# Kernel optimization log

Measured on AMD Instinct MI355X. Metric: run time of the kernel, lower is better.

The kernel has to match this reference:

```python
import jax, jax.numpy as jnp
import numpy as np

B, QL, VL, HID, NH, CH = 16, 512, 512, 1024, 4, 10
DIM = HID // NH  # 256


def setup_inputs() -> dict:
    key = jax.random.key(0)
    ks = jax.random.split(key, 16)
    n = lambda k, s, sc=0.02: jax.random.normal(k, s, jnp.float32) * sc
    return {
        "query": jax.random.normal(ks[0], (B, QL, HID), jnp.float32),
        "value": jax.random.normal(ks[1], (B, VL, HID), jnp.float32),
        "prev_attn": jax.nn.softmax(jax.random.normal(ks[2], (B * NH, VL), jnp.float32), axis=-1),
        "conv_w": n(ks[3], (CH, 1, 3)),          # conv1d weight (out, in, k)
        "conv_b": jnp.zeros((CH,), jnp.float32),
        "Wq": n(ks[4], (HID, HID)), "bq": jnp.zeros((HID,), jnp.float32),  # query_projection
        "Wv": n(ks[5], (HID, HID)),               # value_projection (no bias)
        "Wloc": n(ks[6], (CH, DIM)),              # loc_projection (no bias)
        "bias": jax.random.uniform(ks[7], (HID,), jnp.float32, -0.1, 0.1),
        "Wout": n(ks[8], (2 * HID, HID)), "bout": jnp.zeros((HID,), jnp.float32),
        "swq": n(ks[9], (DIM, DIM)), "sbq": jnp.zeros((DIM,), jnp.float32),
        "swk": n(ks[10], (DIM, DIM)), "sbk": jnp.zeros((DIM,), jnp.float32),
        "swv": n(ks[11], (DIM, DIM)), "sbv": jnp.zeros((DIM,), jnp.float32),
    }


def _forward(query, value, prev_attn, conv_w, conv_b, Wq, bq, Wv, Wloc, bias,
             Wout, bout, swq, sbq, swk, sbk, swv, sbv):
    # location energy: conv1d over prev alignment, then per-head linear
    conv = jax.lax.conv_general_dilated(
        prev_attn[:, None, :], conv_w, window_strides=(1,), padding=((1, 1),),
        dimension_numbers=("NCH", "OIH", "NCH")) + conv_b[None, :, None]  # (B*NH, CH, VL)
    conv = conv.reshape(B, NH, CH, VL).transpose(0, 1, 3, 2)              # (B, NH, VL, CH)
    loc = jnp.einsum("bhvc,cd->bhvd", conv, Wloc)                         # (B, NH, VL, DIM)
    loc = loc.transpose(0, 2, 1, 3).reshape(B, VL, HID)                   # (B, VL, HID)

    q = query @ Wq + bq                                                   # (B, QL, HID)
    v = value @ Wv + loc + bias                                           # (B, VL, HID)

    # split heads: (B, L, NH, DIM) -> (NH*B, L, DIM)
    qh = q.reshape(B, QL, NH, DIM).transpose(2, 0, 1, 3).reshape(NH * B, QL, DIM)
    vh = v.reshape(B, VL, NH, DIM).transpose(2, 0, 1, 3).reshape(NH * B, VL, DIM)

    # scaled dot-product attention with key = value = vh (intended call)
    qq = qh @ swq + sbq
    kk = vh @ swk + sbk
    vv = vh @ swv + sbv
    scores = jnp.einsum("nqd,nkd->nqk", qq, kk) / np.float32(np.sqrt(DIM))
    attn = jax.nn.softmax(scores, axis=-1)                                # (NH*B, QL, VL)
    ctx = jnp.einsum("nqk,nkd->nqd", attn, vv)

    # merge heads: (NH, B, QL, DIM) -> (B, QL, HID)
    ctx = ctx.reshape(NH, B, QL, DIM).transpose(1, 2, 0, 3).reshape(B, QL, HID)

    combined = jnp.concatenate([ctx, query], axis=2)                      # (B, QL, 2*HID)
    out = jnp.tanh(combined @ Wout + bout)                                # (B, QL, HID)
    return out, attn


def reference(query, value, prev_attn, conv_w, conv_b, Wq, bq, Wv, Wloc, bias,
              Wout, bout, swq, sbq, swk, sbk, swv, sbv):
    return _forward(query, value, prev_attn, conv_w, conv_b, Wq, bq, Wv, Wloc,
                    bias, Wout, bout, swq, sbq, swk, sbk, swv, sbv)
```

## Files before the change

kernel.cpp:

```cpp
#include <hip/hip_runtime.h>
#include <math.h>

#define B_   16
#define QL_  512
#define VL_  512
#define HID_ 1024
#define NH_  4
#define CH_  10
#define DIM_ 256

typedef __attribute__((ext_vector_type(4))) float f32x4;
typedef __attribute__((ext_vector_type(8))) short bf16x8;

__device__ __forceinline__ ushort f2bf(float f) {
    union { float f; uint32_t u; } c; c.f = f;
    uint32_t u = c.u;
    u += 0x7fffu + ((u >> 16) & 1u);
    return (ushort)(u >> 16);
}

__device__ __forceinline__ void gload16(const void* g, void* l) {
    __builtin_amdgcn_global_load_lds((const __attribute__((address_space(1))) void*)g,
                                     (__attribute__((address_space(3))) void*)l,
                                     16, 0, 0);
}

__global__ __launch_bounds__(256)
void gemm_bf16(const ushort* __restrict__ A, const ushort* __restrict__ Bt,
               void* __restrict__ Cv, void* __restrict__ Cv2,
               const float* __restrict__ bias,
               int K, int lda, int ldb, int ldc,
               long long a1, long long a2, long long b1, long long b2,
               long long c1, long long c2, int WB,
               float post_scale, int flags)
{
    __shared__ ushort As[2][128 * 64];
    __shared__ ushort Bs[2][128 * 64];

    int z = blockIdx.z;
    int zm = z % WB, zd = z / WB;
    A  += a1 * zm + a2 * zd;
    Bt += b1 * zm + b2 * zd;
    long long coff = c1 * (long long)zm + c2 * (long long)zd;

    int gx = gridDim.x;
    int nwg = gx * gridDim.y;
    int flat = blockIdx.y * gx + blockIdx.x;
    int q = nwg >> 3, r = nwg & 7;
    int xcd = flat & 7, idx = flat >> 3;
    int logical = (xcd < r ? xcd * (q + 1) : r * (q + 1) + (xcd - r) * q) + idx;
    int brow = (logical / gx) * 128;
    int bcol = (logical % gx) * 128;

    int t = threadIdx.x;
    int lane = t & 63, w = t >> 6;
    int wr = (w >> 1) * 64, wc = (w & 1) * 64;

    int srow  = t >> 3;
    int sslot = t & 7;
    int sk = ((sslot ^ (srow & 7)) << 3);
    const ushort* gaBase = A  + (long long)(brow + srow) * lda + sk;
    const ushort* gbBase = Bt + (long long)(bcol + srow) * ldb + sk;

    f32x4 acc[4][4] = {};

    auto stage = [&](int buf, int k0) {
        ushort* la = &As[buf][t * 8];
        ushort* lb = &Bs[buf][t * 8];
        #pragma unroll
        for (int i = 0; i < 4; ++i) {
            gload16(gaBase + (long long)(i * 32) * lda + k0, la + i * 2048);
            gload16(gbBase + (long long)(i * 32) * ldb + k0, lb + i * 2048);
        }
    };

    int NT = K >> 6;
    stage(0, 0);
    int cur = 0;
    for (int tI = 0; tI < NT; ++tI) {
        if (tI + 1 < NT) {
            stage(cur ^ 1, (tI + 1) << 6);
            asm volatile("s_waitcnt vmcnt(8)" ::: "memory");
        } else {
            asm volatile("s_waitcnt vmcnt(0)" ::: "memory");
        }
        __builtin_amdgcn_s_barrier();
        __builtin_amdgcn_sched_barrier(0);

        #pragma unroll
        for (int kk = 0; kk < 2; ++kk) {
            int slot = ((kk << 2) + (lane >> 4)) ^ (lane & 7);
            const ushort* ab = &As[cur][(wr + (lane & 15)) * 64 + slot * 8];
            const ushort* bb = &Bs[cur][(wc + (lane & 15)) * 64 + slot * 8];
            bf16x8 af[4], bfr[4];
            #pragma unroll
            for (int m = 0; m < 4; ++m) af[m]  = *(const bf16x8*)(ab + m * 1024);
            #pragma unroll
            for (int n = 0; n < 4; ++n) bfr[n] = *(const bf16x8*)(bb + n * 1024);
            #pragma unroll
            for (int m = 0; m < 4; ++m)
                #pragma unroll
                for (int n = 0; n < 4; ++n)
                    acc[m][n] = __builtin_amdgcn_mfma_f32_16x16x32_bf16(af[m], bfr[n], acc[m][n], 0, 0, 0);
        }

        __builtin_amdgcn_s_barrier();
        __builtin_amdgcn_sched_barrier(0);
        cur ^= 1;
    }

    float*  Cf = (float*)Cv + coff;
    ushort* Cb = (ushort*)Cv + coff;
    ushort* C2 = (ushort*)Cv2;
    #pragma unroll
    for (int m = 0; m < 4; ++m) {
        int r0 = brow + wr + m * 16 + (lane >> 4) * 4;
        #pragma unroll
        for (int n = 0; n < 4; ++n) {
            int c = bcol + wc + n * 16 + (lane & 15);
            float bv = bias ? bias[c] : 0.0f;
            float v0 = (acc[m][n][0] + bv) * post_scale;
            float v1 = (acc[m][n][1] + bv) * post_scale;
            float v2 = (acc[m][n][2] + bv) * post_scale;
            float v3 = (acc[m][n][3] + bv) * post_scale;
            if (flags & 2) { v0 = tanhf(v0); v1 = tanhf(v1); v2 = tanhf(v2); v3 = tanhf(v3); }
            if ((flags & 8) && c >= 1024) {
                ushort4 o;
                o.x = f2bf(v0); o.y = f2bf(v1); o.z = f2bf(v2); o.w = f2bf(v3);
                *(ushort4*)&C2[(long long)(c - 1024) * 8192 + r0] = o;
            } else if (flags & 1) {
                Cb[(long long)(r0 + 0) * ldc + c] = f2bf(v0);
                Cb[(long long)(r0 + 1) * ldc + c] = f2bf(v1);
                Cb[(long long)(r0 + 2) * ldc + c] = f2bf(v2);
                Cb[(long long)(r0 + 3) * ldc + c] = f2bf(v3);
            } else {
                Cf[(long long)(r0 + 0) * ldc + c] = v0;
                Cf[(long long)(r0 + 1) * ldc + c] = v1;
                Cf[(long long)(r0 + 2) * ldc + c] = v2;
                Cf[(long long)(r0 + 3) * ldc + c] = v3;
            }
        }
    }
}

__global__ __launch_bounds__(512, 1)
void scores_softmax(const ushort* __restrict__ qq, const ushort* __restrict__ kk,
                    float* __restrict__ attn, ushort* __restrict__ attnb)
{
    __shared__ ushort As[128 * 32];
    __shared__ ushort Bs[512 * 32];
    __shared__ float redm[4][128];
    __shared__ float reds[4][128];

    int z = blockIdx.z;
    int b = z & 15, h = z >> 4;
    const ushort* Abase = qq + (long long)b * 524288 + h * 256;
    const ushort* Bbase = kk + (long long)b * 524288 + h * 256;
    float*  aout = attn  + (long long)z * 262144;
    ushort* bout = attnb + (long long)z * 262144;

    int brow = blockIdx.y * 128;

    int t = threadIdx.x;
    int lane = t & 63, w = t >> 6;
    int wr = (w >> 2) * 64;
    int wc = (w & 3) * 128;

    int srow = t >> 2, sslot = t & 3;
    int sk = ((sslot ^ ((srow >> 1) & 3)) << 3);
    const ushort* ga = Abase + (long long)(brow + srow) * 1024 + sk;
    const ushort* gb = Bbase + (long long)srow * 1024 + sk;

    f32x4 acc[4][8] = {};

    for (int k0 = 0; k0 < 256; k0 += 32) {
        gload16(ga + k0, &As[t * 8]);
        #pragma unroll
        for (int i = 0; i < 4; ++i)
            gload16(gb + (long long)(i * 128) * 1024 + k0, &Bs[t * 8 + i * 4096]);
        __syncthreads();

        int slot = (lane >> 4) ^ ((lane >> 1) & 3);
        const ushort* ab = &As[(wr + (lane & 15)) * 32 + slot * 8];
        const ushort* bb = &Bs[(wc + (lane & 15)) * 32 + slot * 8];
        bf16x8 af[4], bfr[8];
        #pragma unroll
        for (int m = 0; m < 4; ++m) af[m]  = *(const bf16x8*)(ab + m * 512);
        #pragma unroll
        for (int n = 0; n < 8; ++n) bfr[n] = *(const bf16x8*)(bb + n * 512);
        #pragma unroll
        for (int m = 0; m < 4; ++m)
            #pragma unroll
            for (int n = 0; n < 8; ++n)
                acc[m][n] = __builtin_amdgcn_mfma_f32_16x16x32_bf16(af[m], bfr[n], acc[m][n], 0, 0, 0);
        __syncthreads();
    }

    float rmax[4][4], rinv[4][4];
    #pragma unroll
    for (int m = 0; m < 4; ++m)
        #pragma unroll
        for (int j = 0; j < 4; ++j) {
            float pm = acc[m][0][j];
            #pragma unroll
            for (int n = 1; n < 8; ++n) pm = fmaxf(pm, acc[m][n][j]);
            pm = fmaxf(pm, __shfl_xor(pm, 1));
            pm = fmaxf(pm, __shfl_xor(pm, 2));
            pm = fmaxf(pm, __shfl_xor(pm, 4));
            pm = fmaxf(pm, __shfl_xor(pm, 8));
            if ((lane & 15) == 0)
                redm[w & 3][wr + m * 16 + (lane >> 4) * 4 + j] = pm;
        }
    __syncthreads();
    #pragma unroll
    for (int m = 0; m < 4; ++m)
        #pragma unroll
        for (int j = 0; j < 4; ++j) {
            int row = wr + m * 16 + (lane >> 4) * 4 + j;
            rmax[m][j] = fmaxf(fmaxf(redm[0][row], redm[1][row]),
                               fmaxf(redm[2][row], redm[3][row]));
        }
    #pragma unroll
    for (int m = 0; m < 4; ++m)
        #pragma unroll
        for (int j = 0; j < 4; ++j) {
            float ps = 0.f;
            #pragma unroll
            for (int n = 0; n < 8; ++n) {
                float e = __expf(acc[m][n][j] - rmax[m][j]);
                acc[m][n][j] = e;
                ps += e;
            }
            ps += __shfl_xor(ps, 1);
            ps += __shfl_xor(ps, 2);
            ps += __shfl_xor(ps, 4);
            ps += __shfl_xor(ps, 8);
            if ((lane & 15) == 0)
                reds[w & 3][wr + m * 16 + (lane >> 4) * 4 + j] = ps;
        }
    __syncthreads();
    #pragma unroll
    for (int m = 0; m < 4; ++m)
        #pragma unroll
        for (int j = 0; j < 4; ++j) {
            int row = wr + m * 16 + (lane >> 4) * 4 + j;
            rinv[m][j] = 1.0f / (reds[0][row] + reds[1][row] + reds[2][row] + reds[3][row]);
        }
    #pragma unroll
    for (int m = 0; m < 4; ++m) {
        int r0 = brow + wr + m * 16 + (lane >> 4) * 4;
        #pragma unroll
        for (int n = 0; n < 8; ++n) {
            int c = wc + n * 16 + (lane & 15);
            #pragma unroll
            for (int j = 0; j < 4; ++j) {
                float v = acc[m][n][j] * rinv[m][j];
                aout[(long long)(r0 + j) * 512 + c] = v;
                bout[(long long)(r0 + j) * 512 + c] = f2bf(v);
            }
        }
    }
}

__global__ __launch_bounds__(256)
void vext_fill_conv(const float* __restrict__ prev, const float* __restrict__ cw,
                    const float* __restrict__ cb, ushort* __restrict__ vext)
{
    int idx = blockIdx.x * 256 + threadIdx.x;
    int row = idx >> 6, j = idx & 63;
    int b = row >> 9, l = row & 511;
    ushort v = 0;
    if (j < 40) {
        int h = j / 10, c = j - h * 10;
        const float* p = prev + (long long)(b * 4 + h) * VL_;
        float xm = (l > 0)       ? p[l - 1] : 0.f;
        float x0 = p[l];
        float xp = (l < VL_ - 1) ? p[l + 1] : 0.f;
        v = f2bf(xm * cw[c * 3 + 0] + x0 * cw[c * 3 + 1] + xp * cw[c * 3 + 2] + cb[c]);
    }
    vext[(long long)row * 1088 + 1024 + j] = v;
}

__global__ __launch_bounds__(256)
void fold_small(const float* __restrict__ bq, const float* __restrict__ sbq, const float* __restrict__ swq,
                const float* __restrict__ bias, const float* __restrict__ sbk, const float* __restrict__ swk,
                const float* __restrict__ sbv, const float* __restrict__ swv,
                const float* __restrict__ Wloc,
                float* __restrict__ bqq, float* __restrict__ bkv,
                float* __restrict__ wlK, float* __restrict__ wlV)
{
    int idx = blockIdx.x * 256 + threadIdx.x;
    if (idx < 1024) {
        int h = idx >> 8, d = idx & 255;
        float s = 0.f;
        for (int j = 0; j < 256; ++j) s += bq[h * 256 + j] * swq[j * 256 + d];
        bqq[idx] = s + sbq[d];
    } else if (idx < 3072) {
        int i = idx - 1024;
        int kv = i >> 10, ii = i & 1023;
        int h = ii >> 8, d = ii & 255;
        const float* sw = kv ? swv : swk;
        const float* sb = kv ? sbv : sbk;
        float s = 0.f;
        for (int j = 0; j < 256; ++j) s += bias[h * 256 + j] * sw[j * 256 + d];
        bkv[i] = s + sb[d];
    } else if (idx < 5632) {
        int i = idx - 3072; int c = i >> 8, d = i & 255;
        float s = 0.f;
        for (int j = 0; j < 256; ++j) s += Wloc[c * 256 + j] * swk[j * 256 + d];
        wlK[i] = s;
    } else if (idx < 8192) {
        int i = idx - 5632; int c = i >> 8, d = i & 255;
        float s = 0.f;
        for (int j = 0; j < 256; ++j) s += Wloc[c * 256 + j] * swv[j * 256 + d];
        wlV[i] = s;
    }
}

__global__ __launch_bounds__(256)
void cast_rows(const float* __restrict__ in, ushort* __restrict__ out, int ld_out)
{
    long long idx = (long long)blockIdx.x * 256 + threadIdx.x;
    long long row = idx >> 8;
    int c4 = (int)(idx & 255) * 4;
    float4 v = *(const float4*)&in[row * 1024 + c4];
    ushort4 o;
    o.x = f2bf(v.x); o.y = f2bf(v.y); o.z = f2bf(v.z); o.w = f2bf(v.w);
    *(ushort4*)&out[row * ld_out + c4] = o;
}

__global__ __launch_bounds__(256)
void transpose_cast(const float* __restrict__ in, ushort* __restrict__ out, int R, int C, int ld_out)
{
    __shared__ float tile[64][65];
    int r0 = blockIdx.y * 64, c0 = blockIdx.x * 64;
    int t = threadIdx.x;
    int tr = t >> 2, tc = (t & 3) * 16;
    const float* ip = in + (long long)(r0 + tr) * C + c0 + tc;
    #pragma unroll
    for (int i = 0; i < 4; ++i) {
        float4 v = *(const float4*)(ip + i * 4);
        tile[tr][tc + i * 4 + 0] = v.x;
        tile[tr][tc + i * 4 + 1] = v.y;
        tile[tr][tc + i * 4 + 2] = v.z;
        tile[tr][tc + i * 4 + 3] = v.w;
    }
    __syncthreads();
    int cl = t >> 2, rl = (t & 3) * 16;
    ushort* op = out + (long long)(c0 + cl) * ld_out + r0 + rl;
    #pragma unroll
    for (int i = 0; i < 16; ++i) op[i] = f2bf(tile[rl + i][cl]);
}

__global__ __launch_bounds__(256)
void sw3_transpose(const float* __restrict__ swq, const float* __restrict__ swk,
                   const float* __restrict__ swv, ushort* __restrict__ oq,
                   ushort* __restrict__ ok, ushort* __restrict__ ov)
{
    __shared__ float tile[64][65];
    const float* in = (blockIdx.z == 0) ? swq : (blockIdx.z == 1) ? swk : swv;
    ushort* out     = (blockIdx.z == 0) ? oq  : (blockIdx.z == 1) ? ok  : ov;
    int r0 = blockIdx.y * 64, c0 = blockIdx.x * 64;
    int t = threadIdx.x;
    int tr = t >> 2, tc = (t & 3) * 16;
    const float* ip = in + (long long)(r0 + tr) * 256 + c0 + tc;
    #pragma unroll
    for (int i = 0; i < 4; ++i) {
        float4 v = *(const float4*)(ip + i * 4);
        tile[tr][tc + i * 4 + 0] = v.x;
        tile[tr][tc + i * 4 + 1] = v.y;
        tile[tr][tc + i * 4 + 2] = v.z;
        tile[tr][tc + i * 4 + 3] = v.w;
    }
    __syncthreads();
    int cl = t >> 2, rl = (t & 3) * 16;
    ushort* op = out + (long long)(c0 + cl) * 256 + r0 + rl;
    #pragma unroll
    for (int i = 0; i < 16; ++i) op[i] = f2bf(tile[rl + i][cl]);
}

__global__ __launch_bounds__(256)
void btext_fill(const float* __restrict__ wlK, const float* __restrict__ wlV,
                ushort* __restrict__ btExt)
{
    int idx = blockIdx.x * 256 + threadIdx.x;
    int n = idx >> 6, j = idx & 63;
    ushort v = 0;
    if (j < 40) {
        int hp = j / 10, c = j - hp * 10;
        int nn = n & 1023;
        int h = nn >> 8, d = nn & 255;
        if (hp == h) {
            const float* wl = (n >= 1024) ? wlV : wlK;
            v = f2bf(wl[c * 256 + d]);
        }
    }
    btExt[(long long)n * 1088 + 1024 + j] = v;
}

extern "C" void kernel_launch(void* const* d_in, const int* in_sizes, int n_in,
                              void* d_out, int out_size, void* d_ws, size_t ws_size,
                              hipStream_t stream)
{
    (void)in_sizes; (void)n_in; (void)out_size; (void)ws_size;

    const float* query = (const float*)d_in[0];
    const float* value = (const float*)d_in[1];
    const float* prev  = (const float*)d_in[2];
    const float* convw = (const float*)d_in[3];
    const float* convb = (const float*)d_in[4];
    const float* Wq    = (const float*)d_in[5];
    const float* bq    = (const float*)d_in[6];
    const float* Wv    = (const float*)d_in[7];
    const float* Wloc  = (const float*)d_in[8];
    const float* bias  = (const float*)d_in[9];
    const float* Wout  = (const float*)d_in[10];
    const float* bout  = (const float*)d_in[11];
    const float* swq   = (const float*)d_in[12];
    const float* sbq   = (const float*)d_in[13];
    const float* swk   = (const float*)d_in[14];
    const float* sbk   = (const float*)d_in[15];
    const float* swv   = (const float*)d_in[16];
    const float* sbv   = (const float*)d_in[17];

    float* out_buf  = (float*)d_out;
    float* attn_buf = out_buf + (long long)B_ * QL_ * HID_;

    char* wsb = (char*)d_ws;
    ushort* vext   = (ushort*)(wsb + 0);
    ushort* WoutTb = (ushort*)(wsb + 0);
    ushort* kkb    = (ushort*)(wsb + 17825792);
    ushort* attnb  = (ushort*)(wsb + 34603008);
    ushort* Acat   = (ushort*)(wsb + 68157440);
    ushort* qqb    = (ushort*)(wsb + 101711872);
    ushort* vvT_b  = (ushort*)(wsb + 118489088);
    float*  bqq    = (float*)(wsb + 135266304);
    float*  bkv    = (float*)(wsb + 135270400);
    float*  wlK    = (float*)(wsb + 135278592);
    float*  wlV    = (float*)(wsb + 135288832);
    ushort* swqTb  = (ushort*)(wsb + 135299072);
    ushort* swkTb  = (ushort*)(wsb + 135430144);
    ushort* swvTb  = (ushort*)(wsb + 135561216);
    ushort* Wqb    = (ushort*)(wsb + 135692288);
    ushort* Wvb    = (ushort*)(wsb + 137789440);
    ushort* wqqTb  = (ushort*)(wsb + 139886592);
    ushort* btExt  = (ushort*)(wsb + 141983744);

    fold_small<<<32, 256, 0, stream>>>(bq, sbq, swq, bias, sbk, swk, sbv, swv, Wloc,
                                       bqq, bkv, wlK, wlV);
    vext_fill_conv<<<2048, 256, 0, stream>>>(prev, convw, convb, vext);
    cast_rows<<<1024, 256, 0, stream>>>(Wq, Wqb, 1024);
    cast_rows<<<1024, 256, 0, stream>>>(Wv, Wvb, 1024);
    sw3_transpose<<<dim3(4, 4, 3), 256, 0, stream>>>(swq, swk, swv, swqTb, swkTb, swvTb);
    cast_rows<<<8192, 256, 0, stream>>>(query, Acat + 1024, 2048);
    cast_rows<<<8192, 256, 0, stream>>>(value, vext, 1088);

    gemm_bf16<<<dim3(8, 2, 4), 256, 0, stream>>>(swqTb, Wqb, wqqTb, nullptr, nullptr,
        256, 256, 1024, 1024, 0, 0, 0, 256, 0, 262144, 1, 1.0f, 1);
    gemm_bf16<<<dim3(8, 2, 8), 256, 0, stream>>>(swkTb, Wvb, btExt, nullptr, nullptr,
        256, 256, 1024, 1088, 0, 65536, 256, 0, 278528, 1114112, 4, 1.0f, 1);
    btext_fill<<<512, 256, 0, stream>>>(wlK, wlV, btExt);

    gemm_bf16<<<dim3(8, 64, 1), 256, 0, stream>>>(Acat + 1024, wqqTb, qqb, nullptr, bqq,
        1024, 2048, 1024, 1024, 0, 0, 0, 0, 0, 0, 1, 0.0625f, 1);

    gemm_bf16<<<dim3(16, 64, 1), 256, 0, stream>>>(vext, btExt, kkb, vvT_b, bkv,
        1088, 1088, 1088, 1024, 0, 0, 0, 0, 0, 0, 1, 1.0f, 1 | 8);

    transpose_cast<<<dim3(16, 32), 256, 0, stream>>>(Wout, WoutTb, 2048, 1024, 2048);

    scores_softmax<<<dim3(1, 4, 64), 512, 0, stream>>>(qqb, kkb, attn_buf, attnb);

    gemm_bf16<<<dim3(2, 4, 64), 256, 0, stream>>>(attnb, vvT_b, Acat, nullptr, nullptr,
        512, 512, 8192, 2048,
        262144, 4194304, 512, 2097152, 1048576, 256, 16, 1.0f, 1);

    gemm_bf16<<<dim3(8, 64, 1), 256, 0, stream>>>(Acat, WoutTb, out_buf, nullptr, bout,
        2048, 2048, 2048, 1024, 0, 0, 0, 0, 0, 0, 1, 1.0f, 2);
}
```

Measured before the change: 267.6 us.

## Add 8-wave 256x128 GEMM with XCD remap and fuse prep kernels

Adds a new 512-thread GEMM kernel that uses 256x128 tiles, double-buffered LDS loads, split MFMA phases with setprio and barriers, and a grid remap that groups blocks by XCD. It replaces the three large projection and output GEMMs. Separately, the cast and conv preprocessing launches are merged into two kernels, which cuts launch count. The larger tile per block reduces global traffic per FLOP but lowers occupancy, and the hand-placed barriers add scheduling risk.

```diff
diff --git a/kernel.cpp b/kernel.cpp
--- a/kernel.cpp
+++ b/kernel.cpp
@@ -11,6 +11,7 @@
 
 typedef __attribute__((ext_vector_type(4))) float f32x4;
 typedef __attribute__((ext_vector_type(8))) short bf16x8;
+typedef long long ll;
 
 __device__ __forceinline__ ushort f2bf(float f) {
     union { float f; uint32_t u; } c; c.f = f;
@@ -23,6 +24,120 @@
     __builtin_amdgcn_global_load_lds((const __attribute__((address_space(1))) void*)g,
                                      (__attribute__((address_space(3))) void*)l,
                                      16, 0, 0);
+}
+
+__global__ __launch_bounds__(512)
+void gemm8p(const ushort* __restrict__ A, const ushort* __restrict__ Bt,
+            void* __restrict__ Cv, void* __restrict__ Cv2,
+            const float* __restrict__ bias,
+            int K, int lda, int ldb, int ldc,
+            float post_scale, int flags)
+{
+    __shared__ ushort As[2][256 * 32];
+    __shared__ ushort Bs[2][128 * 32];
+
+    int gx = gridDim.x, nwg = gx * gridDim.y;
+    int flat = blockIdx.y * gx + blockIdx.x;
+    int q = nwg >> 3, r = nwg & 7;
+    int xcd = flat & 7, idx = flat >> 3;
+    int logical = (xcd < r ? xcd * (q + 1) : r * (q + 1) + (xcd - r) * q) + idx;
+    int brow = (logical / gx) * 256;
+    int bcol = (logical % gx) * 128;
+
+    int t = threadIdx.x;
+    int lane = t & 63, w = t >> 6;
+    int wm = w >> 1, wn = w & 1;
+    int wr = wm * 64, wc = wn * 64;
+
+    int srow = t >> 2, slot = t & 3;
+    int sk = ((slot ^ ((srow >> 1) & 3)) << 3);
+    const ushort* gA0 = A  + (ll)(brow + srow) * lda + sk;
+    const ushort* gA1 = A  + (ll)(brow + 128 + srow) * lda + sk;
+    const ushort* gB  = Bt + (ll)(bcol + srow) * ldb + sk;
+
+    f32x4 acc[4][4] = {};
+
+    auto stage = [&](int buf, int k0) {
+        gload16(gA0 + k0, &As[buf][t * 8]);
+        gload16(gA1 + k0, &As[buf][4096 + t * 8]);
+        gload16(gB  + k0, &Bs[buf][t * 8]);
+    };
+
+    int NT = K >> 5;
+    stage(0, 0);
+    __syncthreads();
+    int cur = 0;
+    int slotR = (lane >> 4) ^ ((lane >> 1) & 3);
+    for (int tI = 0; tI < NT; ++tI) {
+        const ushort* ab = &As[cur][(wr + (lane & 15)) * 32 + slotR * 8];
+        const ushort* bb = &Bs[cur][(wc + (lane & 15)) * 32 + slotR * 8];
+
+        bf16x8 af[4], b0, b1;
+        #pragma unroll
+        for (int m = 0; m < 4; ++m) af[m] = *(const bf16x8*)(ab + m * 512);
+        b0 = *(const bf16x8*)(bb);
+        b1 = *(const bf16x8*)(bb + 512);
+        if (tI + 1 < NT) stage(cur ^ 1, (tI + 1) << 5);
+        __builtin_amdgcn_s_barrier();
+        __builtin_amdgcn_sched_barrier(0);
+        __builtin_amdgcn_s_setprio(1);
+        #pragma unroll
+        for (int m = 0; m < 4; ++m) {
+            acc[m][0] = __builtin_amdgcn_mfma_f32_16x16x32_bf16(af[m], b0, acc[m][0], 0, 0, 0);
+            acc[m][1] = __builtin_amdgcn_mfma_f32_16x16x32_bf16(af[m], b1, acc[m][1], 0, 0, 0);
+        }
+        __builtin_amdgcn_s_setprio(0);
+        __builtin_amdgcn_s_barrier();
+        __builtin_amdgcn_sched_barrier(0);
+
+        bf16x8 b2 = *(const bf16x8*)(bb + 1024);
+        bf16x8 b3 = *(const bf16x8*)(bb + 1536);
+        __builtin_amdgcn_s_setprio(1);
+        #pragma unroll
+        for (int m = 0; m < 4; ++m) {
+            acc[m][2] = __builtin_amdgcn_mfma_f32_16x16x32_bf16(af[m], b2, acc[m][2], 0, 0, 0);
+            acc[m][3] = __builtin_amdgcn_mfma_f32_16x16x32_bf16(af[m], b3, acc[m][3], 0, 0, 0);
+        }
+        __builtin_amdgcn_s_setprio(0);
+        if (tI + 1 < NT)
+            asm volatile("s_waitcnt vmcnt(0)" ::: "memory");
+        __builtin_amdgcn_s_barrier();
+        __builtin_amdgcn_sched_barrier(0);
+        cur ^= 1;
+    }
+
+    float*  Cf = (float*)Cv;
+    ushort* Cb = (ushort*)Cv;
+    ushort* C2 = (ushort*)Cv2;
+    #pragma unroll
+    for (int m = 0; m < 4; ++m) {
+        int r0 = brow + wr + m * 16 + (lane >> 4) * 4;
+        #pragma unroll
+        for (int n = 0; n < 4; ++n) {
+            int c = bcol + wc + n * 16 + (lane & 15);
+            float bv = bias ? bias[c] : 0.0f;
+            float v0 = (acc[m][n][0] + bv) * post_scale;
+            float v1 = (acc[m][n][1] + bv) * post_scale;
+            float v2 = (acc[m][n][2] + bv) * post_scale;
+            float v3 = (acc[m][n][3] + bv) * post_scale;
+            if (flags & 2) { v0 = tanhf(v0); v1 = tanhf(v1); v2 = tanhf(v2); v3 = tanhf(v3); }
+            if ((flags & 8) && c >= 1024) {
+                ushort4 o;
+                o.x = f2bf(v0); o.y = f2bf(v1); o.z = f2bf(v2); o.w = f2bf(v3);
+                *(ushort4*)&C2[(ll)(c - 1024) * 8192 + r0] = o;
+            } else if (flags & 1) {
+                Cb[(ll)(r0 + 0) * ldc + c] = f2bf(v0);
+                Cb[(ll)(r0 + 1) * ldc + c] = f2bf(v1);
+                Cb[(ll)(r0 + 2) * ldc + c] = f2bf(v2);
+                Cb[(ll)(r0 + 3) * ldc + c] = f2bf(v3);
+            } else {
+                Cf[(ll)(r0 + 0) * ldc + c] = v0;
+                Cf[(ll)(r0 + 1) * ldc + c] = v1;
+                Cf[(ll)(r0 + 2) * ldc + c] = v2;
+                Cf[(ll)(r0 + 3) * ldc + c] = v3;
+            }
+        }
+    }
 }
 
 __global__ __launch_bounds__(256)
@@ -154,10 +269,10 @@
 
     int z = blockIdx.z;
     int b = z & 15, h = z >> 4;
-    const ushort* Abase = qq + (long long)b * 524288 + h * 256;
-    const ushort* Bbase = kk + (long long)b * 524288 + h * 256;
-    float*  aout = attn  + (long long)z * 262144;
-    ushort* bout = attnb + (long long)z * 262144;
+    const ushort* Abase = qq + (ll)b * 524288 + h * 256;
+    const ushort* Bbase = kk + (ll)b * 524288 + h * 256;
+    float*  aout = attn  + (ll)z * 262144;
+    ushort* bout = attnb + (ll)z * 262144;
 
     int brow = blockIdx.y * 128;
 
@@ -168,8 +283,8 @@
 
     int srow = t >> 2, sslot = t & 3;
     int sk = ((sslot ^ ((srow >> 1) & 3)) << 3);
-    const ushort* ga = Abase + (long long)(brow + srow) * 1024 + sk;
-    const ushort* gb = Bbase + (long long)srow * 1024 + sk;
+    const ushort* ga = Abase + (ll)(brow + srow) * 1024 + sk;
+    const ushort* gb = Bbase + (ll)srow * 1024 + sk;
 
     f32x4 acc[4][8] = {};
 
@@ -177,7 +292,7 @@
         gload16(ga + k0, &As[t * 8]);
         #pragma unroll
         for (int i = 0; i < 4; ++i)
-            gload16(gb + (long long)(i * 128) * 1024 + k0, &Bs[t * 8 + i * 4096]);
+            gload16(gb + (ll)(i * 128) * 1024 + k0, &Bs[t * 8 + i * 4096]);
         __syncthreads();
 
         int slot = (lane >> 4) ^ ((lane >> 1) & 3);
@@ -255,41 +370,72 @@
             #pragma unroll
             for (int j = 0; j < 4; ++j) {
                 float v = acc[m][n][j] * rinv[m][j];
-                aout[(long long)(r0 + j) * 512 + c] = v;
-                bout[(long long)(r0 + j) * 512 + c] = f2bf(v);
+                aout[(ll)(r0 + j) * 512 + c] = v;
+                bout[(ll)(r0 + j) * 512 + c] = f2bf(v);
             }
         }
     }
 }
 
 __global__ __launch_bounds__(256)
-void vext_fill_conv(const float* __restrict__ prev, const float* __restrict__ cw,
-                    const float* __restrict__ cb, ushort* __restrict__ vext)
-{
-    int idx = blockIdx.x * 256 + threadIdx.x;
-    int row = idx >> 6, j = idx & 63;
-    int b = row >> 9, l = row & 511;
-    ushort v = 0;
-    if (j < 40) {
-        int h = j / 10, c = j - h * 10;
-        const float* p = prev + (long long)(b * 4 + h) * VL_;
-        float xm = (l > 0)       ? p[l - 1] : 0.f;
-        float x0 = p[l];
-        float xp = (l < VL_ - 1) ? p[l + 1] : 0.f;
-        v = f2bf(xm * cw[c * 3 + 0] + x0 * cw[c * 3 + 1] + xp * cw[c * 3 + 2] + cb[c]);
-    }
-    vext[(long long)row * 1088 + 1024 + j] = v;
+void prep_acts(const float* __restrict__ query, const float* __restrict__ value,
+               const float* __restrict__ prev, const float* __restrict__ cw,
+               const float* __restrict__ cb,
+               ushort* __restrict__ Acat, ushort* __restrict__ vext)
+{
+    int bI = blockIdx.x;
+    if (bI < 16384) {
+        const float* in = (bI < 8192) ? query : value;
+        ushort* out = (bI < 8192) ? Acat : vext;
+        int ld_out = (bI < 8192) ? 2048 : 1088;
+        ll idx = (ll)(bI & 8191) * 256 + threadIdx.x;
+        ll row = idx >> 8;
+        int c4 = (int)(idx & 255) * 4;
+        float4 v = *(const float4*)&in[row * 1024 + c4];
+        ushort4 o;
+        o.x = f2bf(v.x); o.y = f2bf(v.y); o.z = f2bf(v.z); o.w = f2bf(v.w);
+        *(ushort4*)&out[row * ld_out + c4] = o;
+    } else {
+        int idx = (bI - 16384) * 256 + threadIdx.x;
+        int row = idx >> 6, j = idx & 63;
+        int b = row >> 9, l = row & 511;
+        ushort v = 0;
+        if (j < 40) {
+            int h = j / 10, c = j - h * 10;
+            const float* p = prev + (ll)(b * 4 + h) * VL_;
+            float xm = (l > 0)       ? p[l - 1] : 0.f;
+            float x0 = p[l];
+            float xp = (l < VL_ - 1) ? p[l + 1] : 0.f;
+            v = f2bf(xm * cw[c * 3 + 0] + x0 * cw[c * 3 + 1] + xp * cw[c * 3 + 2] + cb[c]);
+        }
+        vext[(ll)row * 1088 + 1024 + j] = v;
+    }
 }
 
 __global__ __launch_bounds__(256)
-void fold_small(const float* __restrict__ bq, const float* __restrict__ sbq, const float* __restrict__ swq,
-                const float* __restrict__ bias, const float* __restrict__ sbk, const float* __restrict__ swk,
-                const float* __restrict__ sbv, const float* __restrict__ swv,
-                const float* __restrict__ Wloc,
-                float* __restrict__ bqq, float* __restrict__ bkv,
-                float* __restrict__ wlK, float* __restrict__ wlV)
-{
-    int idx = blockIdx.x * 256 + threadIdx.x;
+void prep_w(const float* __restrict__ Wq, const float* __restrict__ Wv,
+            ushort* __restrict__ Wqb, ushort* __restrict__ Wvb,
+            const float* __restrict__ bq, const float* __restrict__ sbq, const float* __restrict__ swq,
+            const float* __restrict__ bias, const float* __restrict__ sbk, const float* __restrict__ swk,
+            const float* __restrict__ sbv, const float* __restrict__ swv,
+            const float* __restrict__ Wloc,
+            float* __restrict__ bqq, float* __restrict__ bkv,
+            float* __restrict__ wlK, float* __restrict__ wlV)
+{
+    int bI = blockIdx.x;
+    if (bI < 2048) {
+        const float* in = (bI < 1024) ? Wq : Wv;
+        ushort* out = (bI < 1024) ? Wqb : Wvb;
+        ll idx = (ll)(bI & 1023) * 256 + threadIdx.x;
+        ll row = idx >> 8;
+        int c4 = (int)(idx & 255) * 4;
+        float4 v = *(const float4*)&in[row * 1024 + c4];
+        ushort4 o;
+        o.x = f2bf(v.x); o.y = f2bf(v.y); o.z = f2bf(v.z); o.w = f2bf(v.w);
+        *(ushort4*)&out[row * 1024 + c4] = o;
+        return;
+    }
+    int idx = (bI - 2048) * 256 + threadIdx.x;
     if (idx < 1024) {
         int h = idx >> 8, d = idx & 255;
         float s = 0.f;
@@ -318,25 +464,13 @@
 }
 
 __global__ __launch_bounds__(256)
-void cast_rows(const float* __restrict__ in, ushort* __restrict__ out, int ld_out)
-{
-    long long idx = (long long)blockIdx.x * 256 + threadIdx.x;
-    long long row = idx >> 8;
-    int c4 = (int)(idx & 255) * 4;
-    float4 v = *(const float4*)&in[row * 1024 + c4];
-    ushort4 o;
-    o.x = f2bf(v.x); o.y = f2bf(v.y); o.z = f2bf(v.z); o.w = f2bf(v.w);
-    *(ushort4*)&out[row * ld_out + c4] = o;
-}
-
-__global__ __launch_bounds__(256)
 void transpose_cast(const float* __restrict__ in, ushort* __restrict__ out, int R, int C, int ld_out)
 {
     __shared__ float tile[64][65];
     int r0 = blockIdx.y * 64, c0 = blockIdx.x * 64;
     int t = threadIdx.x;
     int tr = t >> 2, tc = (t & 3) * 16;
-    const float* ip = in + (long long)(r0 + tr) * C + c0 + tc;
+    const float* ip = in + (ll)(r0 + tr) * C + c0 + tc;
     #pragma unroll
     for (int i = 0; i < 4; ++i) {
         float4 v = *(const float4*)(ip + i * 4);
@@ -347,7 +481,7 @@
     }
     __syncthreads();
     int cl = t >> 2, rl = (t & 3) * 16;
-    ushort* op = out + (long long)(c0 + cl) * ld_out + r0 + rl;
+    ushort* op = out + (ll)(c0 + cl) * ld_out + r0 + rl;
     #pragma unroll
     for (int i = 0; i < 16; ++i) op[i] = f2bf(tile[rl + i][cl]);
 }
@@ -363,7 +497,7 @@
     int r0 = blockIdx.y * 64, c0 = blockIdx.x * 64;
     int t = threadIdx.x;
     int tr = t >> 2, tc = (t & 3) * 16;
-    const float* ip = in + (long long)(r0 + tr) * 256 + c0 + tc;
+    const float* ip = in + (ll)(r0 + tr) * 256 + c0 + tc;
     #pragma unroll
     for (int i = 0; i < 4; ++i) {
         float4 v = *(const float4*)(ip + i * 4);
@@ -374,7 +508,7 @@
     }
     __syncthreads();
     int cl = t >> 2, rl = (t & 3) * 16;
-    ushort* op = out + (long long)(c0 + cl) * 256 + r0 + rl;
+    ushort* op = out + (ll)(c0 + cl) * 256 + r0 + rl;
     #pragma unroll
     for (int i = 0; i < 16; ++i) op[i] = f2bf(tile[rl + i][cl]);
 }
@@ -395,7 +529,7 @@
             v = f2bf(wl[c * 256 + d]);
         }
     }
-    btExt[(long long)n * 1088 + 1024 + j] = v;
+    btExt[(ll)n * 1088 + 1024 + j] = v;
 }
 
 extern "C" void kernel_launch(void* const* d_in, const int* in_sizes, int n_in,
@@ -424,7 +558,7 @@
     const float* sbv   = (const float*)d_in[17];
 
     float* out_buf  = (float*)d_out;
-    float* attn_buf = out_buf + (long long)B_ * QL_ * HID_;
+    float* attn_buf = out_buf + (ll)B_ * QL_ * HID_;
 
     char* wsb = (char*)d_ws;
     ushort* vext   = (ushort*)(wsb + 0);
@@ -446,14 +580,10 @@
     ushort* wqqTb  = (ushort*)(wsb + 139886592);
     ushort* btExt  = (ushort*)(wsb + 141983744);
 
-    fold_small<<<32, 256, 0, stream>>>(bq, sbq, swq, bias, sbk, swk, sbv, swv, Wloc,
-                                       bqq, bkv, wlK, wlV);
-    vext_fill_conv<<<2048, 256, 0, stream>>>(prev, convw, convb, vext);
-    cast_rows<<<1024, 256, 0, stream>>>(Wq, Wqb, 1024);
-    cast_rows<<<1024, 256, 0, stream>>>(Wv, Wvb, 1024);
+    prep_acts<<<18432, 256, 0, stream>>>(query, value, prev, convw, convb, Acat + 1024, vext);
+    prep_w<<<2080, 256, 0, stream>>>(Wq, Wv, Wqb, Wvb, bq, sbq, swq, bias, sbk, swk,
+                                     sbv, swv, Wloc, bqq, bkv, wlK, wlV);
     sw3_transpose<<<dim3(4, 4, 3), 256, 0, stream>>>(swq, swk, swv, swqTb, swkTb, swvTb);
-    cast_rows<<<8192, 256, 0, stream>>>(query, Acat + 1024, 2048);
-    cast_rows<<<8192, 256, 0, stream>>>(value, vext, 1088);
 
     gemm_bf16<<<dim3(8, 2, 4), 256, 0, stream>>>(swqTb, Wqb, wqqTb, nullptr, nullptr,
         256, 256, 1024, 1024, 0, 0, 0, 256, 0, 262144, 1, 1.0f, 1);
@@ -461,11 +591,11 @@
         256, 256, 1024, 1088, 0, 65536, 256, 0, 278528, 1114112, 4, 1.0f, 1);
     btext_fill<<<512, 256, 0, stream>>>(wlK, wlV, btExt);
 
-    gemm_bf16<<<dim3(8, 64, 1), 256, 0, stream>>>(Acat + 1024, wqqTb, qqb, nullptr, bqq,
-        1024, 2048, 1024, 1024, 0, 0, 0, 0, 0, 0, 1, 0.0625f, 1);
-
-    gemm_bf16<<<dim3(16, 64, 1), 256, 0, stream>>>(vext, btExt, kkb, vvT_b, bkv,
-        1088, 1088, 1088, 1024, 0, 0, 0, 0, 0, 0, 1, 1.0f, 1 | 8);
+    gemm8p<<<dim3(8, 32), 512, 0, stream>>>(Acat + 1024, wqqTb, qqb, nullptr, bqq,
+        1024, 2048, 1024, 1024, 0.0625f, 1);
+
+    gemm8p<<<dim3(16, 32), 512, 0, stream>>>(vext, btExt, kkb, vvT_b, bkv,
+        1088, 1088, 1088, 1024, 1.0f, 1 | 8);
 
     transpose_cast<<<dim3(16, 32), 256, 0, stream>>>(Wout, WoutTb, 2048, 1024, 2048);
 
@@ -475,6 +605,6 @@
         512, 512, 8192, 2048,
         262144, 4194304, 512, 2097152, 1048576, 256, 16, 1.0f, 1);
 
-    gemm_bf16<<<dim3(8, 64, 1), 256, 0, stream>>>(Acat, WoutTb, out_buf, nullptr, bout,
-        2048, 2048, 2048, 1024, 0, 0, 0, 0, 0, 0, 1, 1.0f, 2);
-}
+    gemm8p<<<dim3(8, 32), 512, 0, stream>>>(Acat, WoutTb, out_buf, nullptr, bout,
+        2048, 2048, 2048, 1024, 1.0f, 2);
+}
```

Result: slower. 273.4 us (+2.2%).

## Double-buffer LDS in scores_softmax and merge prep kernels into fewer launches

Applied to the files above, without the earlier changes.

The scores_softmax K-loop now uses two LDS buffers. The next tile's global-to-LDS loads are issued before computing the current tile, with explicit vmcnt waits and raw barriers in place of __syncthreads. Separately, the small cast, conv and fold kernels are merged into two launches (prep_acts, prep_w) to cut launch overhead. The double buffer doubles LDS use in a kernel already bound to one block per CU, and the hand-tuned vmcnt count must match the five loads issued per stage.

```diff
diff --git a/kernel.cpp b/kernel.cpp
--- a/kernel.cpp
+++ b/kernel.cpp
@@ -11,6 +11,7 @@
 
 typedef __attribute__((ext_vector_type(4))) float f32x4;
 typedef __attribute__((ext_vector_type(8))) short bf16x8;
+typedef long long ll;
 
 __device__ __forceinline__ ushort f2bf(float f) {
     union { float f; uint32_t u; } c; c.f = f;
@@ -147,17 +148,17 @@
 void scores_softmax(const ushort* __restrict__ qq, const ushort* __restrict__ kk,
                     float* __restrict__ attn, ushort* __restrict__ attnb)
 {
-    __shared__ ushort As[128 * 32];
-    __shared__ ushort Bs[512 * 32];
+    __shared__ ushort As[2][128 * 32];
+    __shared__ ushort Bs[2][512 * 32];
     __shared__ float redm[4][128];
     __shared__ float reds[4][128];
 
     int z = blockIdx.z;
     int b = z & 15, h = z >> 4;
-    const ushort* Abase = qq + (long long)b * 524288 + h * 256;
-    const ushort* Bbase = kk + (long long)b * 524288 + h * 256;
-    float*  aout = attn  + (long long)z * 262144;
-    ushort* bout = attnb + (long long)z * 262144;
+    const ushort* Abase = qq + (ll)b * 524288 + h * 256;
+    const ushort* Bbase = kk + (ll)b * 524288 + h * 256;
+    float*  aout = attn  + (ll)z * 262144;
+    ushort* bout = attnb + (ll)z * 262144;
 
     int brow = blockIdx.y * 128;
 
@@ -168,21 +169,34 @@
 
     int srow = t >> 2, sslot = t & 3;
     int sk = ((sslot ^ ((srow >> 1) & 3)) << 3);
-    const ushort* ga = Abase + (long long)(brow + srow) * 1024 + sk;
-    const ushort* gb = Bbase + (long long)srow * 1024 + sk;
+    const ushort* ga = Abase + (ll)(brow + srow) * 1024 + sk;
+    const ushort* gb = Bbase + (ll)srow * 1024 + sk;
 
     f32x4 acc[4][8] = {};
 
-    for (int k0 = 0; k0 < 256; k0 += 32) {
-        gload16(ga + k0, &As[t * 8]);
+    auto stage = [&](int buf, int k0) {
+        gload16(ga + k0, &As[buf][t * 8]);
         #pragma unroll
         for (int i = 0; i < 4; ++i)
-            gload16(gb + (long long)(i * 128) * 1024 + k0, &Bs[t * 8 + i * 4096]);
-        __syncthreads();
+            gload16(gb + (ll)(i * 128) * 1024 + k0, &Bs[buf][t * 8 + i * 4096]);
+    };
+
+    int cur = 0;
+    stage(0, 0);
+    #pragma unroll
+    for (int tI = 0; tI < 8; ++tI) {
+        if (tI + 1 < 8) {
+            stage(cur ^ 1, (tI + 1) << 5);
+            asm volatile("s_waitcnt vmcnt(5)" ::: "memory");
+        } else {
+            asm volatile("s_waitcnt vmcnt(0)" ::: "memory");
+        }
+        __builtin_amdgcn_s_barrier();
+        __builtin_amdgcn_sched_barrier(0);
 
         int slot = (lane >> 4) ^ ((lane >> 1) & 3);
-        const ushort* ab = &As[(wr + (lane & 15)) * 32 + slot * 8];
-        const ushort* bb = &Bs[(wc + (lane & 15)) * 32 + slot * 8];
+        const ushort* ab = &As[cur][(wr + (lane & 15)) * 32 + slot * 8];
+        const ushort* bb = &Bs[cur][(wc + (lane & 15)) * 32 + slot * 8];
         bf16x8 af[4], bfr[8];
         #pragma unroll
         for (int m = 0; m < 4; ++m) af[m]  = *(const bf16x8*)(ab + m * 512);
@@ -193,7 +207,10 @@
             #pragma unroll
             for (int n = 0; n < 8; ++n)
                 acc[m][n] = __builtin_amdgcn_mfma_f32_16x16x32_bf16(af[m], bfr[n], acc[m][n], 0, 0, 0);
-        __syncthreads();
+
+        __builtin_amdgcn_s_barrier();
+        __builtin_amdgcn_sched_barrier(0);
+        cur ^= 1;
     }
 
     float rmax[4][4], rinv[4][4];
@@ -255,41 +272,72 @@
             #pragma unroll
             for (int j = 0; j < 4; ++j) {
                 float v = acc[m][n][j] * rinv[m][j];
-                aout[(long long)(r0 + j) * 512 + c] = v;
-                bout[(long long)(r0 + j) * 512 + c] = f2bf(v);
+                aout[(ll)(r0 + j) * 512 + c] = v;
+                bout[(ll)(r0 + j) * 512 + c] = f2bf(v);
             }
         }
     }
 }
 
 __global__ __launch_bounds__(256)
-void vext_fill_conv(const float* __restrict__ prev, const float* __restrict__ cw,
-                    const float* __restrict__ cb, ushort* __restrict__ vext)
-{
-    int idx = blockIdx.x * 256 + threadIdx.x;
-    int row = idx >> 6, j = idx & 63;
-    int b = row >> 9, l = row & 511;
-    ushort v = 0;
-    if (j < 40) {
-        int h = j / 10, c = j - h * 10;
-        const float* p = prev + (long long)(b * 4 + h) * VL_;
-        float xm = (l > 0)       ? p[l - 1] : 0.f;
-        float x0 = p[l];
-        float xp = (l < VL_ - 1) ? p[l + 1] : 0.f;
-        v = f2bf(xm * cw[c * 3 + 0] + x0 * cw[c * 3 + 1] + xp * cw[c * 3 + 2] + cb[c]);
-    }
-    vext[(long long)row * 1088 + 1024 + j] = v;
+void prep_acts(const float* __restrict__ query, const float* __restrict__ value,
+               const float* __restrict__ prev, const float* __restrict__ cw,
+               const float* __restrict__ cb,
+               ushort* __restrict__ Acat, ushort* __restrict__ vext)
+{
+    int bI = blockIdx.x;
+    if (bI < 16384) {
+        const float* in = (bI < 8192) ? query : value;
+        ushort* out = (bI < 8192) ? Acat : vext;
+        int ld_out = (bI < 8192) ? 2048 : 1088;
+        ll idx = (ll)(bI & 8191) * 256 + threadIdx.x;
+        ll row = idx >> 8;
+        int c4 = (int)(idx & 255) * 4;
+        float4 v = *(const float4*)&in[row * 1024 + c4];
+        ushort4 o;
+        o.x = f2bf(v.x); o.y = f2bf(v.y); o.z = f2bf(v.z); o.w = f2bf(v.w);
+        *(ushort4*)&out[row * ld_out + c4] = o;
+    } else {
+        int idx = (bI - 16384) * 256 + threadIdx.x;
+        int row = idx >> 6, j = idx & 63;
+        int b = row >> 9, l = row & 511;
+        ushort v = 0;
+        if (j < 40) {
+            int h = j / 10, c = j - h * 10;
+            const float* p = prev + (ll)(b * 4 + h) * VL_;
+            float xm = (l > 0)       ? p[l - 1] : 0.f;
+            float x0 = p[l];
+            float xp = (l < VL_ - 1) ? p[l + 1] : 0.f;
+            v = f2bf(xm * cw[c * 3 + 0] + x0 * cw[c * 3 + 1] + xp * cw[c * 3 + 2] + cb[c]);
+        }
+        vext[(ll)row * 1088 + 1024 + j] = v;
+    }
 }
 
 __global__ __launch_bounds__(256)
-void fold_small(const float* __restrict__ bq, const float* __restrict__ sbq, const float* __restrict__ swq,
-                const float* __restrict__ bias, const float* __restrict__ sbk, const float* __restrict__ swk,
-                const float* __restrict__ sbv, const float* __restrict__ swv,
-                const float* __restrict__ Wloc,
-                float* __restrict__ bqq, float* __restrict__ bkv,
-                float* __restrict__ wlK, float* __restrict__ wlV)
-{
-    int idx = blockIdx.x * 256 + threadIdx.x;
+void prep_w(const float* __restrict__ Wq, const float* __restrict__ Wv,
+            ushort* __restrict__ Wqb, ushort* __restrict__ Wvb,
+            const float* __restrict__ bq, const float* __restrict__ sbq, const float* __restrict__ swq,
+            const float* __restrict__ bias, const float* __restrict__ sbk, const float* __restrict__ swk,
+            const float* __restrict__ sbv, const float* __restrict__ swv,
+            const float* __restrict__ Wloc,
+            float* __restrict__ bqq, float* __restrict__ bkv,
+            float* __restrict__ wlK, float* __restrict__ wlV)
+{
+    int bI = blockIdx.x;
+    if (bI < 2048) {
+        const float* in = (bI < 1024) ? Wq : Wv;
+        ushort* out = (bI < 1024) ? Wqb : Wvb;
+        ll idx = (ll)(bI & 1023) * 256 + threadIdx.x;
+        ll row = idx >> 8;
+        int c4 = (int)(idx & 255) * 4;
+        float4 v = *(const float4*)&in[row * 1024 + c4];
+        ushort4 o;
+        o.x = f2bf(v.x); o.y = f2bf(v.y); o.z = f2bf(v.z); o.w = f2bf(v.w);
+        *(ushort4*)&out[row * 1024 + c4] = o;
+        return;
+    }
+    int idx = (bI - 2048) * 256 + threadIdx.x;
     if (idx < 1024) {
         int h = idx >> 8, d = idx & 255;
         float s = 0.f;
@@ -318,25 +366,13 @@
 }
 
 __global__ __launch_bounds__(256)
-void cast_rows(const float* __restrict__ in, ushort* __restrict__ out, int ld_out)
-{
-    long long idx = (long long)blockIdx.x * 256 + threadIdx.x;
-    long long row = idx >> 8;
-    int c4 = (int)(idx & 255) * 4;
-    float4 v = *(const float4*)&in[row * 1024 + c4];
-    ushort4 o;
-    o.x = f2bf(v.x); o.y = f2bf(v.y); o.z = f2bf(v.z); o.w = f2bf(v.w);
-    *(ushort4*)&out[row * ld_out + c4] = o;
-}
-
-__global__ __launch_bounds__(256)
 void transpose_cast(const float* __restrict__ in, ushort* __restrict__ out, int R, int C, int ld_out)
 {
     __shared__ float tile[64][65];
     int r0 = blockIdx.y * 64, c0 = blockIdx.x * 64;
     int t = threadIdx.x;
     int tr = t >> 2, tc = (t & 3) * 16;
-    const float* ip = in + (long long)(r0 + tr) * C + c0 + tc;
+    const float* ip = in + (ll)(r0 + tr) * C + c0 + tc;
     #pragma unroll
     for (int i = 0; i < 4; ++i) {
         float4 v = *(const float4*)(ip + i * 4);
@@ -347,7 +383,7 @@
     }
     __syncthreads();
     int cl = t >> 2, rl = (t & 3) * 16;
-    ushort* op = out + (long long)(c0 + cl) * ld_out + r0 + rl;
+    ushort* op = out + (ll)(c0 + cl) * ld_out + r0 + rl;
     #pragma unroll
     for (int i = 0; i < 16; ++i) op[i] = f2bf(tile[rl + i][cl]);
 }
@@ -363,7 +399,7 @@
     int r0 = blockIdx.y * 64, c0 = blockIdx.x * 64;
     int t = threadIdx.x;
     int tr = t >> 2, tc = (t & 3) * 16;
-    const float* ip = in + (long long)(r0 + tr) * 256 + c0 + tc;
+    const float* ip = in + (ll)(r0 + tr) * 256 + c0 + tc;
     #pragma unroll
     for (int i = 0; i < 4; ++i) {
         float4 v = *(const float4*)(ip + i * 4);
@@ -374,7 +410,7 @@
     }
     __syncthreads();
     int cl = t >> 2, rl = (t & 3) * 16;
-    ushort* op = out + (long long)(c0 + cl) * 256 + r0 + rl;
+    ushort* op = out + (ll)(c0 + cl) * 256 + r0 + rl;
     #pragma unroll
     for (int i = 0; i < 16; ++i) op[i] = f2bf(tile[rl + i][cl]);
 }
@@ -395,7 +431,7 @@
             v = f2bf(wl[c * 256 + d]);
         }
     }
-    btExt[(long long)n * 1088 + 1024 + j] = v;
+    btExt[(ll)n * 1088 + 1024 + j] = v;
 }
 
 extern "C" void kernel_launch(void* const* d_in, const int* in_sizes, int n_in,
@@ -424,7 +460,7 @@
     const float* sbv   = (const float*)d_in[17];
 
     float* out_buf  = (float*)d_out;
-    float* attn_buf = out_buf + (long long)B_ * QL_ * HID_;
+    float* attn_buf = out_buf + (ll)B_ * QL_ * HID_;
 
     char* wsb = (char*)d_ws;
     ushort* vext   = (ushort*)(wsb + 0);
@@ -446,14 +482,10 @@
     ushort* wqqTb  = (ushort*)(wsb + 139886592);
     ushort* btExt  = (ushort*)(wsb + 141983744);
 
-    fold_small<<<32, 256, 0, stream>>>(bq, sbq, swq, bias, sbk, swk, sbv, swv, Wloc,
-                                       bqq, bkv, wlK, wlV);
-    vext_fill_conv<<<2048, 256, 0, stream>>>(prev, convw, convb, vext);
-    cast_rows<<<1024, 256, 0, stream>>>(Wq, Wqb, 1024);
-    cast_rows<<<1024, 256, 0, stream>>>(Wv, Wvb, 1024);
+    prep_acts<<<18432, 256, 0, stream>>>(query, value, prev, convw, convb, Acat + 1024, vext);
+    prep_w<<<2080, 256, 0, stream>>>(Wq, Wv, Wqb, Wvb, bq, sbq, swq, bias, sbk, swk,
+                                     sbv, swv, Wloc, bqq, bkv, wlK, wlV);
     sw3_transpose<<<dim3(4, 4, 3), 256, 0, stream>>>(swq, swk, swv, swqTb, swkTb, swvTb);
-    cast_rows<<<8192, 256, 0, stream>>>(query, Acat + 1024, 2048);
-    cast_rows<<<8192, 256, 0, stream>>>(value, vext, 1088);
 
     gemm_bf16<<<dim3(8, 2, 4), 256, 0, stream>>>(swqTb, Wqb, wqqTb, nullptr, nullptr,
         256, 256, 1024, 1024, 0, 0, 0, 256, 0, 262144, 1, 1.0f, 1);
```

Measured after the change: 261.8 us (median of 2 runs). 1.02x faster.
